# Kernel tuning notes

Hardware: AMD Instinct MI355X
Metric: run time of the kernel (lower is better)

## Reference

```python
import jax, jax.numpy as jnp
import numpy as np

B, C, H, W, WS, SH, NH, P = 64, 512, 28, 28, 7, 3, 16, 10
MLP_H = 2048
EPS = 1e-5
NW = (H // WS) * (W // WS)  # 16 windows per image
N = P + WS * WS             # 59 tokens per window
HEAD_D = C // NH
SCALE = HEAD_D ** -0.5


def _rel_pos_index(ws):
    coords = np.stack(np.meshgrid(np.arange(ws), np.arange(ws), indexing='ij')).reshape(2, -1)
    rel = (coords[:, :, None] - coords[:, None, :]).transpose(1, 2, 0)
    rel[..., 0] += ws - 1
    rel[..., 1] += ws - 1
    rel[..., 0] *= 2 * ws - 1
    return rel.sum(-1)  # (ws*ws, ws*ws)


def _attn_mask(h, w, ws, shift):
    img = np.zeros((h, w), dtype=np.float32)
    slices = (slice(0, -ws), slice(-ws, -shift), slice(-shift, None))
    cnt = 0
    for hs in slices:
        for wsl in slices:
            img[hs, wsl] = cnt
            cnt += 1
    mw = img.reshape(h // ws, ws, w // ws, ws).transpose(0, 2, 1, 3).reshape(-1, ws * ws)
    diff = mw[:, None, :] - mw[:, :, None]
    return np.where(diff != 0, -100.0, 0.0).astype(np.float32)  # (nW, ws*ws, ws*ws)


_RPI = jnp.asarray(_rel_pos_index(WS))
_MASK = jnp.asarray(_attn_mask(H, W, WS, SH))


def _ln(x, g, b):
    mu = jnp.mean(x, -1, keepdims=True)
    var = jnp.mean((x - mu) ** 2, -1, keepdims=True)
    return (x - mu) * jax.lax.rsqrt(var + EPS) * g + b


def _window_partition(x, ws):
    b, h, w, c = x.shape
    x = x.reshape(b, h // ws, ws, w // ws, ws, c).transpose(0, 1, 3, 2, 4, 5)
    return x.reshape(-1, ws, ws, c)


def _window_reverse(win, ws, h, w):
    b = win.shape[0] // ((h // ws) * (w // ws))
    x = win.reshape(b, h // ws, w // ws, ws, ws, -1).transpose(0, 1, 3, 2, 4, 5)
    return x.reshape(b, h, w, -1)


def setup_inputs() -> dict:
    key = jax.random.key(0)
    ks = jax.random.split(key, 8)
    d = {
        'x': jax.random.normal(ks[0], (B, P + H * W, C), jnp.float32),
        'g1': jnp.ones((C,), jnp.float32),
        'b1': jnp.zeros((C,), jnp.float32),
        'qkv_w': jax.random.normal(ks[1], (3 * C, C), jnp.float32) * 0.02,
        'qkv_b': jnp.zeros((3 * C,), jnp.float32),
        'rpb_table': jax.random.normal(ks[2], ((2 * WS - 1) ** 2, NH), jnp.float32) * 0.02,
        'proj_w': jax.random.normal(ks[3], (C, C), jnp.float32) * 0.02,
        'proj_b': jnp.zeros((C,), jnp.float32),
        'g2': jnp.ones((C,), jnp.float32),
        'b2': jnp.zeros((C,), jnp.float32),
        'fc1_w': jax.random.normal(ks[4], (MLP_H, C), jnp.float32) * 0.02,
        'fc1_b': jnp.zeros((MLP_H,), jnp.float32),
        'fc2_w': jax.random.normal(ks[5], (C, MLP_H), jnp.float32) * 0.02,
        'fc2_b': jnp.zeros((C,), jnp.float32),
    }
    return d


def _block(x, g1, b1, qkv_w, qkv_b, rpb_table, proj_w, proj_b, g2, b2, fc1_w, fc1_b, fc2_w, fc2_b):
    prompt = x[:, :P, :]                       # (B, P, C)
    x = x[:, P:, :]                            # (B, H*W, C)
    shortcut = x
    xn = _ln(x, g1, b1).reshape(B, H, W, C)
    # cyclic shift
    xn = jnp.roll(xn, shift=(-SH, -SH), axis=(1, 2))
    xw = _window_partition(xn, WS).reshape(-1, WS * WS, C)  # (B*nW, 49, C)
    # prompt padding (matches torch expand(nW,...).reshape order: index = w*B + b)
    pw = jnp.broadcast_to(prompt[None], (NW, B, P, C)).reshape(-1, P, C)
    xw = jnp.concatenate([pw, xw], axis=1)     # (B*nW, N, C)
    B_ = B * NW
    # attention
    qkv = (xw @ qkv_w.T + qkv_b).reshape(B_, N, 3, NH, HEAD_D).transpose(2, 0, 3, 1, 4)
    q, k, v = qkv[0], qkv[1], qkv[2]
    attn = jnp.einsum('bhnd,bhmd->bhnm', q * SCALE, k)  # (B_, NH, N, N)
    bias = rpb_table[_RPI.reshape(-1)].reshape(WS * WS, WS * WS, NH).transpose(2, 0, 1)
    bias = jnp.pad(bias, ((0, 0), (P, 0), (P, 0)))       # (NH, N, N)
    mask = jnp.pad(_MASK, ((0, 0), (P, 0), (P, 0)))      # (nW, N, N)
    attn = attn + bias[None]
    attn = attn.reshape(B, NW, NH, N, N) + mask[None, :, None]
    attn = jax.nn.softmax(attn.reshape(B_, NH, N, N), axis=-1)
    out = jnp.einsum('bhnm,bhmd->bhnd', attn, v).transpose(0, 2, 1, 3).reshape(B_, N, C)
    out = out @ proj_w.T + proj_b
    # drop prompts, un-window, un-shift
    out = out[:, P:, :].reshape(-1, WS, WS, C)
    xs = _window_reverse(out, WS, H, W)
    xs = jnp.roll(xs, shift=(SH, SH), axis=(1, 2)).reshape(B, H * W, C)
    x = shortcut + xs
    # MLP (exact GELU, as torch nn.GELU)
    h = _ln(x, g2, b2)
    h = jax.nn.gelu(h @ fc1_w.T + fc1_b, approximate=False)
    h = h @ fc2_w.T + fc2_b
    return x + h


def reference(x, g1, b1, qkv_w, qkv_b, rpb_table, proj_w, proj_b, g2, b2, fc1_w, fc1_b, fc2_w, fc2_b):
    return _block(x, g1, b1, qkv_w, qkv_b, rpb_table, proj_w, proj_b, g2, b2, fc1_w, fc1_b, fc2_w, fc2_b)
```

## Files before the change

### kernel.cpp

```cpp
#include <hip/hip_runtime.h>
#include <stdint.h>

typedef unsigned short u16;
typedef unsigned int u32;
typedef __attribute__((ext_vector_type(8))) short short8;
typedef __attribute__((ext_vector_type(4))) float f32x4;

__device__ __forceinline__ u16 f2bf(float f) {
  u32 u = __builtin_bit_cast(u32, f);
  u32 r = u + 0x7FFFu + ((u >> 16) & 1u);
  return (u16)(r >> 16);
}

__device__ __forceinline__ void gl_lds16(const void* g, void* l) {
  __builtin_amdgcn_global_load_lds((__attribute__((address_space(1))) void*)g,
                                   (__attribute__((address_space(3))) void*)l,
                                   16, 0, 0);
}

__device__ __forceinline__ float gelu_fast(float v) {
  float u = 0.7978845608028654f * (v + 0.044715f * v * v * v);
  float a = fabsf(u);
  float e = __expf(-2.0f * a);
  float t = (1.0f - e) / (1.0f + e);
  float th = copysignf(t, u);
  return 0.5f * v * (1.0f + th);
}

__global__ __launch_bounds__(256) void cvt_bf16(const float* __restrict__ in,
                                                u16* __restrict__ out, int n4) {
  int idx = blockIdx.x * 256 + threadIdx.x;
  if (idx < n4) {
    float4 v = ((const float4*)in)[idx];
    u32 lo = (u32)f2bf(v.x) | ((u32)f2bf(v.y) << 16);
    u32 hi = (u32)f2bf(v.z) | ((u32)f2bf(v.w) << 16);
    ((uint2*)out)[idx] = make_uint2(lo, hi);
  }
}

__global__ __launch_bounds__(256) void ln1_kernel(const float* __restrict__ x,
                                                  const float* __restrict__ g,
                                                  const float* __restrict__ bta,
                                                  u16* __restrict__ xcat) {
  int wave = threadIdx.x >> 6, lane = threadIdx.x & 63;
  int row = blockIdx.x * 4 + wave;
  const float* src;
  bool do_ln;
  if (row < 640) {
    int bb = row / 10, p = row - bb * 10;
    src = x + ((size_t)bb * 794 + p) * 512;
    do_ln = false;
  } else {
    int r2 = row - 640;
    int i = r2 / 49, t = r2 - i * 49;
    int bb = i >> 4, nw = i & 15;
    int tr = t / 7, tc = t - tr * 7;
    int hh = (nw >> 2) * 7 + tr + 3; if (hh >= 28) hh -= 28;
    int ww = (nw & 3) * 7 + tc + 3;  if (ww >= 28) ww -= 28;
    src = x + ((size_t)bb * 794 + 10 + hh * 28 + ww) * 512;
    do_ln = true;
  }
  float4 v0 = ((const float4*)src)[lane * 2];
  float4 v1 = ((const float4*)src)[lane * 2 + 1];
  float vals[8] = {v0.x, v0.y, v0.z, v0.w, v1.x, v1.y, v1.z, v1.w};
  u16 ob[8];
  if (do_ln) {
    float s = 0.f, s2 = 0.f;
#pragma unroll
    for (int j = 0; j < 8; ++j) { s += vals[j]; s2 += vals[j] * vals[j]; }
#pragma unroll
    for (int o = 32; o > 0; o >>= 1) { s += __shfl_xor(s, o); s2 += __shfl_xor(s2, o); }
    float mu = s * (1.0f / 512.0f);
    float var = s2 * (1.0f / 512.0f) - mu * mu;
    float inv = rsqrtf(var + 1e-5f);
    float4 ga = ((const float4*)g)[lane * 2], gb = ((const float4*)g)[lane * 2 + 1];
    float4 ba = ((const float4*)bta)[lane * 2], bb2 = ((const float4*)bta)[lane * 2 + 1];
    float gv[8] = {ga.x, ga.y, ga.z, ga.w, gb.x, gb.y, gb.z, gb.w};
    float bv[8] = {ba.x, ba.y, ba.z, ba.w, bb2.x, bb2.y, bb2.z, bb2.w};
#pragma unroll
    for (int j = 0; j < 8; ++j) ob[j] = f2bf((vals[j] - mu) * inv * gv[j] + bv[j]);
  } else {
#pragma unroll
    for (int j = 0; j < 8; ++j) ob[j] = f2bf(vals[j]);
  }
  u32 w0 = (u32)ob[0] | ((u32)ob[1] << 16);
  u32 w1 = (u32)ob[2] | ((u32)ob[3] << 16);
  u32 w2 = (u32)ob[4] | ((u32)ob[5] << 16);
  u32 w3 = (u32)ob[6] | ((u32)ob[7] << 16);
  ((uint4*)(xcat + (size_t)row * 512))[lane] = make_uint4(w0, w1, w2, w3);
}

__global__ __launch_bounds__(256) void ln2_kernel(const float* __restrict__ xn,
                                                  const float* __restrict__ g,
                                                  const float* __restrict__ bta,
                                                  u16* __restrict__ outb) {
  int wave = threadIdx.x >> 6, lane = threadIdx.x & 63;
  size_t row = (size_t)blockIdx.x * 4 + wave;
  const float* src = xn + row * 512;
  float4 v0 = ((const float4*)src)[lane * 2];
  float4 v1 = ((const float4*)src)[lane * 2 + 1];
  float vals[8] = {v0.x, v0.y, v0.z, v0.w, v1.x, v1.y, v1.z, v1.w};
  float s = 0.f, s2 = 0.f;
#pragma unroll
  for (int j = 0; j < 8; ++j) { s += vals[j]; s2 += vals[j] * vals[j]; }
#pragma unroll
  for (int o = 32; o > 0; o >>= 1) { s += __shfl_xor(s, o); s2 += __shfl_xor(s2, o); }
  float mu = s * (1.0f / 512.0f);
  float var = s2 * (1.0f / 512.0f) - mu * mu;
  float inv = rsqrtf(var + 1e-5f);
  float4 ga = ((const float4*)g)[lane * 2], gb = ((const float4*)g)[lane * 2 + 1];
  float4 ba = ((const float4*)bta)[lane * 2], bb2 = ((const float4*)bta)[lane * 2 + 1];
  float gv[8] = {ga.x, ga.y, ga.z, ga.w, gb.x, gb.y, gb.z, gb.w};
  float bv[8] = {ba.x, ba.y, ba.z, ba.w, bb2.x, bb2.y, bb2.z, bb2.w};
  u16 ob[8];
#pragma unroll
  for (int j = 0; j < 8; ++j) ob[j] = f2bf((vals[j] - mu) * inv * gv[j] + bv[j]);
  u32 w0 = (u32)ob[0] | ((u32)ob[1] << 16);
  u32 w1 = (u32)ob[2] | ((u32)ob[3] << 16);
  u32 w2 = (u32)ob[4] | ((u32)ob[5] << 16);
  u32 w3 = (u32)ob[6] | ((u32)ob[7] << 16);
  ((uint4*)(outb + row * 512))[lane] = make_uint4(w0, w1, w2, w3);
}

template <int EPI>
__global__ __launch_bounds__(256) void gemm128d(const u16* __restrict__ A,
                                                const u16* __restrict__ Wt,
                                                const float* __restrict__ bias,
                                                u16* __restrict__ outb,
                                                float* __restrict__ outf,
                                                const float* __restrict__ res,
                                                int M, int N, int K, int Ntiles) {
  __shared__ __align__(16) u16 Asm[2][128 * 32];
  __shared__ __align__(16) u16 Bsm[2][128 * 32];
  const int tid = threadIdx.x;
  const int lane = tid & 63;
  const int wv = tid >> 6;
  const int wm = wv >> 1, wn = wv & 1;
  const int lr = lane & 15;
  const int qh = lane >> 4;
  const int swz8 = (qh ^ ((lr >> 1) & 3)) << 3;

  const int nwg = gridDim.x;
  const int qx = nwg >> 3, rx = nwg & 7;
  const int xcd = blockIdx.x & 7, local = blockIdx.x >> 3;
  const int swz = (xcd < rx ? xcd * (qx + 1) : rx * (qx + 1) + (xcd - rx) * qx) + local;
  const int mt = swz / Ntiles, nt = swz - mt * Ntiles;
  const int tm = mt << 7, tn = nt << 7;

  f32x4 acc[4][4];
#pragma unroll
  for (int m = 0; m < 4; ++m)
#pragma unroll
    for (int n = 0; n < 4; ++n)
#pragma unroll
      for (int e = 0; e < 4; ++e) acc[m][n][e] = 0.f;

  const int sr = tid >> 2;
  const int sl = tid & 3;
  const int scol = (sl ^ ((sr >> 1) & 3)) << 3;
  const u16* Ap0 = A + (size_t)(tm + sr) * K + scol;
  const u16* Ap1 = A + (size_t)(tm + 64 + sr) * K + scol;
  const u16* Bp0 = Wt + (size_t)(tn + sr) * K + scol;
  const u16* Bp1 = Wt + (size_t)(tn + 64 + sr) * K + scol;

#define STAGE(buf, k0)                            \
  do {                                            \
    u16* da = &Asm[buf][tid * 8];                 \
    u16* db = &Bsm[buf][tid * 8];                 \
    gl_lds16(Ap0 + (k0), da);                     \
    gl_lds16(Ap1 + (k0), da + 2048);              \
    gl_lds16(Bp0 + (k0), db);                     \
    gl_lds16(Bp1 + (k0), db + 2048);              \
  } while (0)

  const int NT = K >> 5;
  STAGE(0, 0);

  int cur = 0;
  for (int t = 0; t < NT; ++t) {
    if (t + 1 < NT) {
      STAGE(cur ^ 1, (t + 1) << 5);
      asm volatile("s_waitcnt vmcnt(4)" ::: "memory");
    } else {
      asm volatile("s_waitcnt vmcnt(0)" ::: "memory");
    }
    __builtin_amdgcn_s_barrier();
    asm volatile("" ::: "memory");

    const u16* Ab = &Asm[cur][0];
    const u16* Bb = &Bsm[cur][0];
    short8 av[4], bv[4];
#pragma unroll
    for (int m = 0; m < 4; ++m)
      av[m] = *(const short8*)&Ab[(wm * 64 + m * 16 + lr) * 32 + swz8];
#pragma unroll
    for (int n = 0; n < 4; ++n)
      bv[n] = *(const short8*)&Bb[(wn * 64 + n * 16 + lr) * 32 + swz8];
    __builtin_amdgcn_s_setprio(1);
#pragma unroll
    for (int m = 0; m < 4; ++m)
#pragma unroll
      for (int n = 0; n < 4; ++n)
        acc[m][n] = __builtin_amdgcn_mfma_f32_16x16x32_bf16(av[m], bv[n], acc[m][n], 0, 0, 0);
    __builtin_amdgcn_s_setprio(0);
    asm volatile("" ::: "memory");
    __builtin_amdgcn_s_barrier();
    cur ^= 1;
  }
#undef STAGE

  float bcol[4];
#pragma unroll
  for (int n = 0; n < 4; ++n) bcol[n] = bias[tn + wn * 64 + n * 16 + lr];

#pragma unroll
  for (int m = 0; m < 4; ++m) {
#pragma unroll
    for (int r2 = 0; r2 < 4; ++r2) {
      int grow = tm + wm * 64 + m * 16 + qh * 4 + r2;
      if (EPI == 1) {
        int i = grow / 49, t = grow - i * 49;
        int bb = i >> 4, nw = i & 15;
        int tr = t / 7, tc = t - tr * 7;
        int hh = (nw >> 2) * 7 + tr + 3; if (hh >= 28) hh -= 28;
        int ww = (nw & 3) * 7 + tc + 3;  if (ww >= 28) ww -= 28;
        size_t dstr = ((size_t)bb * 784 + hh * 28 + ww) * 512;
        size_t srcr = ((size_t)bb * 794 + 10 + hh * 28 + ww) * 512;
#pragma unroll
        for (int n = 0; n < 4; ++n) {
          int gcol = tn + wn * 64 + n * 16 + lr;
          float v = acc[m][n][r2] + bcol[n];
          outf[dstr + gcol] = v + res[srcr + gcol];
        }
      } else {
#pragma unroll
        for (int n = 0; n < 4; ++n) {
          int gcol = tn + wn * 64 + n * 16 + lr;
          float v = acc[m][n][r2] + bcol[n];
          if (EPI == 0) {
            outb[(size_t)grow * N + gcol] = f2bf(v);
          } else if (EPI == 2) {
            outb[(size_t)grow * N + gcol] = f2bf(gelu_fast(v));
          } else {
            outf[(size_t)grow * N + gcol] = v + res[(size_t)grow * 512 + gcol];
          }
        }
      }
    }
  }
}

__global__ __launch_bounds__(64) void attn_kernel(const u16* __restrict__ Y,
                                                  const float* __restrict__ rpb,
                                                  u16* __restrict__ outp) {
  __shared__ __align__(16) u16 Plds[64 * 64];
  __shared__ __align__(16) u16 Vt[32 * 64];
  __shared__ float biasl[169];
  const int lane = threadIdx.x;
  const int i = blockIdx.x >> 4;
  const int hd = blockIdx.x & 15;
  const int bp = i & 63;
  const int nw = i & 15;
  const int hi = nw >> 2, wi = nw & 3;
  const int lr = lane & 15;
  const int lk = (lane >> 4) * 8;

  for (int j = lane; j < 169; j += 64) biasl[j] = rpb[j * 16 + hd];

  short8 qf[4], kf[4];
#pragma unroll
  for (int m = 0; m < 4; ++m) {
    int t = m * 16 + lr;
    size_t r = (t < 10) ? (size_t)(bp * 10 + t) : (size_t)(640 + i * 49 + (t - 10));
    const u16* base = Y + r * 1536 + hd * 32 + lk;
    if (t < 59) {
      qf[m] = *(const short8*)(base);
      kf[m] = *(const short8*)(base + 512);
    } else {
#pragma unroll
      for (int e = 0; e < 8; ++e) { qf[m][e] = 0; kf[m][e] = 0; }
    }
  }
  {
    int t = lane;
    if (t < 59) {
      size_t r = (t < 10) ? (size_t)(bp * 10 + t) : (size_t)(640 + i * 49 + (t - 10));
      const u16* vp = Y + r * 1536 + 1024 + hd * 32;
      short8 vv0 = *(const short8*)(vp);
      short8 vv1 = *(const short8*)(vp + 8);
      short8 vv2 = *(const short8*)(vp + 16);
      short8 vv3 = *(const short8*)(vp + 24);
#pragma unroll
      for (int e = 0; e < 8; ++e) {
        Vt[e * 64 + t] = (u16)vv0[e];
        Vt[(8 + e) * 64 + t] = (u16)vv1[e];
        Vt[(16 + e) * 64 + t] = (u16)vv2[e];
        Vt[(24 + e) * 64 + t] = (u16)vv3[e];
      }
    } else {
      for (int d = 0; d < 32; ++d) Vt[d * 64 + t] = 0;
    }
  }

  f32x4 s[4][4];
#pragma unroll
  for (int m = 0; m < 4; ++m)
#pragma unroll
    for (int n = 0; n < 4; ++n)
#pragma unroll
      for (int r2 = 0; r2 < 4; ++r2) s[m][n][r2] = 0.f;
#pragma unroll
  for (int m = 0; m < 4; ++m)
#pragma unroll
    for (int n = 0; n < 4; ++n)
      s[m][n] = __builtin_amdgcn_mfma_f32_16x16x32_bf16(qf[m], kf[n], s[m][n], 0, 0, 0);

  __syncthreads();

  const float SCALE = 0.17677669529663687f;
  const int rgrp = lane >> 4;
#pragma unroll
  for (int m = 0; m < 4; ++m) {
#pragma unroll
    for (int r2 = 0; r2 < 4; ++r2) {
      int rn = m * 16 + rgrp * 4 + r2;
      int qa = rn - 10;
      int qra = qa / 7, qca = qa - qra * 7;
      int regA = 0;
      if (qa >= 0 && qa < 49) {
        int ha = hi * 7 + qra, wa = wi * 7 + qca;
        regA = (ha < 21 ? 0 : (ha < 25 ? 1 : 2)) * 3 + (wa < 21 ? 0 : (wa < 25 ? 1 : 2));
      }
      float vloc[4];
      float mx = -3.0e38f;
#pragma unroll
      for (int n = 0; n < 4; ++n) {
        int cm = n * 16 + lr;
        float v;
        if (cm >= 59) {
          v = -3.0e38f;
        } else {
          v = s[m][n][r2] * SCALE;
          if (rn >= 10 && rn < 59 && cm >= 10) {
            int kb = cm - 10;
            int krb = kb / 7, kcb = kb - krb * 7;
            v += biasl[(qra - krb + 6) * 13 + (qca - kcb + 6)];
            int hb = hi * 7 + krb, wb = wi * 7 + kcb;
            int regB = (hb < 21 ? 0 : (hb < 25 ? 1 : 2)) * 3 + (wb < 21 ? 0 : (wb < 25 ? 1 : 2));
            if (regA != regB) v -= 100.0f;
          }
        }
        vloc[n] = v;
        mx = fmaxf(mx, v);
      }
#pragma unroll
      for (int o = 8; o > 0; o >>= 1) mx = fmaxf(mx, __shfl_xor(mx, o));
      float sum = 0.f;
#pragma unroll
      for (int n = 0; n < 4; ++n) {
        float e = __expf(vloc[n] - mx);
        vloc[n] = e;
        sum += e;
      }
#pragma unroll
      for (int o = 8; o > 0; o >>= 1) sum += __shfl_xor(sum, o);
      float inv = 1.0f / sum;
#pragma unroll
      for (int n = 0; n < 4; ++n)
        Plds[rn * 64 + n * 16 + lr] = f2bf(vloc[n] * inv);
    }
  }

  __syncthreads();

  f32x4 o[4][2];
#pragma unroll
  for (int m = 0; m < 4; ++m)
#pragma unroll
    for (int j = 0; j < 2; ++j)
#pragma unroll
      for (int r2 = 0; r2 < 4; ++r2) o[m][j][r2] = 0.f;
#pragma unroll
  for (int ks = 0; ks < 2; ++ks) {
    short8 pf[4], vf[2];
#pragma unroll
    for (int m = 0; m < 4; ++m)
      pf[m] = *(const short8*)&Plds[(m * 16 + lr) * 64 + ks * 32 + lk];
#pragma unroll
    for (int j = 0; j < 2; ++j)
      vf[j] = *(const short8*)&Vt[(j * 16 + lr) * 64 + ks * 32 + lk];
#pragma unroll
    for (int m = 0; m < 4; ++m)
#pragma unroll
      for (int j = 0; j < 2; ++j)
        o[m][j] = __builtin_amdgcn_mfma_f32_16x16x32_bf16(pf[m], vf[j], o[m][j], 0, 0, 0);
  }

#pragma unroll
  for (int m = 0; m < 4; ++m) {
#pragma unroll
    for (int r2 = 0; r2 < 4; ++r2) {
      int rn = m * 16 + rgrp * 4 + r2;
      if (rn >= 10 && rn < 59) {
        size_t row = (size_t)i * 49 + (rn - 10);
        u16* op = outp + row * 512 + hd * 32;
        op[lr] = f2bf(o[m][0][r2]);
        op[16 + lr] = f2bf(o[m][1][r2]);
      }
    }
  }
}

extern "C" void kernel_launch(void* const* d_in, const int* in_sizes, int n_in,
                              void* d_out, int out_size, void* d_ws, size_t ws_size,
                              hipStream_t stream) {
  const float* x = (const float*)d_in[0];
  const float* g1 = (const float*)d_in[1];
  const float* b1 = (const float*)d_in[2];
  const float* qkv_w = (const float*)d_in[3];
  const float* qkv_b = (const float*)d_in[4];
  const float* rpb = (const float*)d_in[5];
  const float* proj_w = (const float*)d_in[6];
  const float* proj_b = (const float*)d_in[7];
  const float* g2 = (const float*)d_in[8];
  const float* b2 = (const float*)d_in[9];
  const float* fc1_w = (const float*)d_in[10];
  const float* fc1_b = (const float*)d_in[11];
  const float* fc2_w = (const float*)d_in[12];
  const float* fc2_b = (const float*)d_in[13];
  float* out = (float*)d_out;

  char* ws = (char*)d_ws;
  u16* qkv_wb = (u16*)(ws + 0);
  u16* proj_wb = (u16*)(ws + 1572864);
  u16* fc1_wb = (u16*)(ws + 2097152);
  u16* fc2_wb = (u16*)(ws + 4194304);
  u16* xcat = (u16*)(ws + 6291456);
  u16* y = (u16*)(ws + 58327040);
  u16* attnv = (u16*)(ws + 214433792);
  float* xnew = (float*)(ws + 265814016);
  u16* hin = xcat;
  u16* hmid = y;

  cvt_bf16<<<768, 256, 0, stream>>>(qkv_w, qkv_wb, 196608);
  cvt_bf16<<<256, 256, 0, stream>>>(proj_w, proj_wb, 65536);
  cvt_bf16<<<1024, 256, 0, stream>>>(fc1_w, fc1_wb, 262144);
  cvt_bf16<<<1024, 256, 0, stream>>>(fc2_w, fc2_wb, 262144);

  ln1_kernel<<<12704, 256, 0, stream>>>(x, g1, b1, xcat);

  gemm128d<0><<<397 * 12, 256, 0, stream>>>(xcat, qkv_wb, qkv_b, y, nullptr, nullptr,
                                            50816, 1536, 512, 12);

  attn_kernel<<<16384, 64, 0, stream>>>(y, rpb, attnv);

  gemm128d<1><<<392 * 4, 256, 0, stream>>>(attnv, proj_wb, proj_b, nullptr, xnew, x,
                                           50176, 512, 512, 4);

  ln2_kernel<<<12544, 256, 0, stream>>>(xnew, g2, b2, hin);

  gemm128d<2><<<392 * 16, 256, 0, stream>>>(hin, fc1_wb, fc1_b, hmid, nullptr, nullptr,
                                            50176, 2048, 512, 16);

  gemm128d<3><<<392 * 4, 256, 0, stream>>>(hmid, fc2_wb, fc2_b, nullptr, out, xnew,
                                           50176, 512, 2048, 4);
}
```

Baseline: 730.4 us.

## Enlarge GEMM block tile to 256x128 with each wave owning a 64x128 slab

The GEMM kernel's block tile grows from 128x128 to 256x128. Each of the four waves now computes a full 64x128 output slab, so every B fragment read from LDS feeds more MFMAs and the weight tiles are loaded half as often per output. Grid sizes are halved to match. A row guard covers the partial last M tile of the QKV GEMM, whose A loads run past the xcat buffer into other workspace memory. The cost is a doubled accumulator footprint (128 floats per lane) and more LDS per block, which may lower occupancy.

```diff
diff --git a/kernel.cpp b/kernel.cpp
--- a/kernel.cpp
+++ b/kernel.cpp
@@ -123,19 +123,18 @@
 }
 
 template <int EPI>
-__global__ __launch_bounds__(256) void gemm128d(const u16* __restrict__ A,
-                                                const u16* __restrict__ Wt,
-                                                const float* __restrict__ bias,
-                                                u16* __restrict__ outb,
-                                                float* __restrict__ outf,
-                                                const float* __restrict__ res,
-                                                int M, int N, int K, int Ntiles) {
-  __shared__ __align__(16) u16 Asm[2][128 * 32];
+__global__ __launch_bounds__(256) void gemmW(const u16* __restrict__ A,
+                                             const u16* __restrict__ Wt,
+                                             const float* __restrict__ bias,
+                                             u16* __restrict__ outb,
+                                             float* __restrict__ outf,
+                                             const float* __restrict__ res,
+                                             int M, int N, int K, int Ntiles) {
+  __shared__ __align__(16) u16 Asm[2][256 * 32];
   __shared__ __align__(16) u16 Bsm[2][128 * 32];
   const int tid = threadIdx.x;
   const int lane = tid & 63;
   const int wv = tid >> 6;
-  const int wm = wv >> 1, wn = wv & 1;
   const int lr = lane & 15;
   const int qh = lane >> 4;
   const int swz8 = (qh ^ ((lr >> 1) & 3)) << 3;
@@ -145,32 +144,33 @@
   const int xcd = blockIdx.x & 7, local = blockIdx.x >> 3;
   const int swz = (xcd < rx ? xcd * (qx + 1) : rx * (qx + 1) + (xcd - rx) * qx) + local;
   const int mt = swz / Ntiles, nt = swz - mt * Ntiles;
-  const int tm = mt << 7, tn = nt << 7;
-
-  f32x4 acc[4][4];
+  const int tm = mt << 8, tn = nt << 7;
+
+  f32x4 acc[4][8];
 #pragma unroll
   for (int m = 0; m < 4; ++m)
 #pragma unroll
-    for (int n = 0; n < 4; ++n)
+    for (int n = 0; n < 8; ++n)
 #pragma unroll
       for (int e = 0; e < 4; ++e) acc[m][n][e] = 0.f;
 
   const int sr = tid >> 2;
   const int sl = tid & 3;
   const int scol = (sl ^ ((sr >> 1) & 3)) << 3;
-  const u16* Ap0 = A + (size_t)(tm + sr) * K + scol;
-  const u16* Ap1 = A + (size_t)(tm + 64 + sr) * K + scol;
-  const u16* Bp0 = Wt + (size_t)(tn + sr) * K + scol;
-  const u16* Bp1 = Wt + (size_t)(tn + 64 + sr) * K + scol;
+  const u16* Ap = A + (size_t)(tm + sr) * K + scol;
+  const u16* Bp = Wt + (size_t)(tn + sr) * K + scol;
+  const size_t a64 = (size_t)64 * K;
 
 #define STAGE(buf, k0)                            \
   do {                                            \
     u16* da = &Asm[buf][tid * 8];                 \
     u16* db = &Bsm[buf][tid * 8];                 \
-    gl_lds16(Ap0 + (k0), da);                     \
-    gl_lds16(Ap1 + (k0), da + 2048);              \
-    gl_lds16(Bp0 + (k0), db);                     \
-    gl_lds16(Bp1 + (k0), db + 2048);              \
+    gl_lds16(Ap + (k0), da);                      \
+    gl_lds16(Ap + a64 + (k0), da + 2048);         \
+    gl_lds16(Ap + 2 * a64 + (k0), da + 4096);     \
+    gl_lds16(Ap + 3 * a64 + (k0), da + 6144);     \
+    gl_lds16(Bp + (k0), db);                      \
+    gl_lds16(Bp + a64 + (k0), db + 2048);         \
   } while (0)
 
   const int NT = K >> 5;
@@ -180,7 +180,7 @@
   for (int t = 0; t < NT; ++t) {
     if (t + 1 < NT) {
       STAGE(cur ^ 1, (t + 1) << 5);
-      asm volatile("s_waitcnt vmcnt(4)" ::: "memory");
+      asm volatile("s_waitcnt vmcnt(6)" ::: "memory");
     } else {
       asm volatile("s_waitcnt vmcnt(0)" ::: "memory");
     }
@@ -189,18 +189,18 @@
 
     const u16* Ab = &Asm[cur][0];
     const u16* Bb = &Bsm[cur][0];
-    short8 av[4], bv[4];
+    short8 av[4], bv[8];
 #pragma unroll
     for (int m = 0; m < 4; ++m)
-      av[m] = *(const short8*)&Ab[(wm * 64 + m * 16 + lr) * 32 + swz8];
-#pragma unroll
-    for (int n = 0; n < 4; ++n)
-      bv[n] = *(const short8*)&Bb[(wn * 64 + n * 16 + lr) * 32 + swz8];
+      av[m] = *(const short8*)&Ab[(wv * 64 + m * 16 + lr) * 32 + swz8];
+#pragma unroll
+    for (int n = 0; n < 8; ++n)
+      bv[n] = *(const short8*)&Bb[(n * 16 + lr) * 32 + swz8];
     __builtin_amdgcn_s_setprio(1);
 #pragma unroll
     for (int m = 0; m < 4; ++m)
 #pragma unroll
-      for (int n = 0; n < 4; ++n)
+      for (int n = 0; n < 8; ++n)
         acc[m][n] = __builtin_amdgcn_mfma_f32_16x16x32_bf16(av[m], bv[n], acc[m][n], 0, 0, 0);
     __builtin_amdgcn_s_setprio(0);
     asm volatile("" ::: "memory");
@@ -209,15 +209,16 @@
   }
 #undef STAGE
 
-  float bcol[4];
-#pragma unroll
-  for (int n = 0; n < 4; ++n) bcol[n] = bias[tn + wn * 64 + n * 16 + lr];
+  float bcol[8];
+#pragma unroll
+  for (int n = 0; n < 8; ++n) bcol[n] = bias[tn + n * 16 + lr];
 
 #pragma unroll
   for (int m = 0; m < 4; ++m) {
 #pragma unroll
     for (int r2 = 0; r2 < 4; ++r2) {
-      int grow = tm + wm * 64 + m * 16 + qh * 4 + r2;
+      int grow = tm + wv * 64 + m * 16 + qh * 4 + r2;
+      if (grow >= M) continue;
       if (EPI == 1) {
         int i = grow / 49, t = grow - i * 49;
         int bb = i >> 4, nw = i & 15;
@@ -227,15 +228,15 @@
         size_t dstr = ((size_t)bb * 784 + hh * 28 + ww) * 512;
         size_t srcr = ((size_t)bb * 794 + 10 + hh * 28 + ww) * 512;
 #pragma unroll
-        for (int n = 0; n < 4; ++n) {
-          int gcol = tn + wn * 64 + n * 16 + lr;
+        for (int n = 0; n < 8; ++n) {
+          int gcol = tn + n * 16 + lr;
           float v = acc[m][n][r2] + bcol[n];
           outf[dstr + gcol] = v + res[srcr + gcol];
         }
       } else {
 #pragma unroll
-        for (int n = 0; n < 4; ++n) {
-          int gcol = tn + wn * 64 + n * 16 + lr;
+        for (int n = 0; n < 8; ++n) {
+          int gcol = tn + n * 16 + lr;
           float v = acc[m][n][r2] + bcol[n];
           if (EPI == 0) {
             outb[(size_t)grow * N + gcol] = f2bf(v);
@@ -449,19 +450,19 @@
 
   ln1_kernel<<<12704, 256, 0, stream>>>(x, g1, b1, xcat);
 
-  gemm128d<0><<<397 * 12, 256, 0, stream>>>(xcat, qkv_wb, qkv_b, y, nullptr, nullptr,
-                                            50816, 1536, 512, 12);
+  gemmW<0><<<199 * 12, 256, 0, stream>>>(xcat, qkv_wb, qkv_b, y, nullptr, nullptr,
+                                         50816, 1536, 512, 12);
 
   attn_kernel<<<16384, 64, 0, stream>>>(y, rpb, attnv);
 
-  gemm128d<1><<<392 * 4, 256, 0, stream>>>(attnv, proj_wb, proj_b, nullptr, xnew, x,
-                                           50176, 512, 512, 4);
+  gemmW<1><<<196 * 4, 256, 0, stream>>>(attnv, proj_wb, proj_b, nullptr, xnew, x,
+                                        50176, 512, 512, 4);
 
   ln2_kernel<<<12544, 256, 0, stream>>>(xnew, g2, b2, hin);
 
-  gemm128d<2><<<392 * 16, 256, 0, stream>>>(hin, fc1_wb, fc1_b, hmid, nullptr, nullptr,
-                                            50176, 2048, 512, 16);
-
-  gemm128d<3><<<392 * 4, 256, 0, stream>>>(hmid, fc2_wb, fc2_b, nullptr, out, xnew,
-                                           50176, 512, 2048, 4);
-}
+  gemmW<2><<<196 * 16, 256, 0, stream>>>(hin, fc1_wb, fc1_b, hmid, nullptr, nullptr,
+                                         50176, 2048, 512, 16);
+
+  gemmW<3><<<196 * 4, 256, 0, stream>>>(hmid, fc2_wb, fc2_b, nullptr, out, xnew,
+                                        50176, 512, 2048, 4);
+}
```

Result: slower. 1.138 ms (+55.8%).

## Load GEMM weight fragments directly from global memory, dropping B LDS staging

Applied to the files above, without the earlier changes.

The GEMM kernel no longer stages the weight (B) tile through shared memory. Each wave now loads its four 16x32 B fragments directly from global memory into registers every K-step, which halves LDS usage and enables a launch-bounds occupancy hint of 3 blocks. The wait counts are adjusted to cover the extra outstanding vector loads. In exchange, B data is no longer shared between the two wm waves through LDS, so each is re-fetched from global memory or L2. The per-lane global reads are 16-byte strided rows, and the B loads have no prefetch ahead of use.

```diff
diff --git a/kernel.cpp b/kernel.cpp
--- a/kernel.cpp
+++ b/kernel.cpp
@@ -123,15 +123,14 @@
 }
 
 template <int EPI>
-__global__ __launch_bounds__(256) void gemm128d(const u16* __restrict__ A,
-                                                const u16* __restrict__ Wt,
-                                                const float* __restrict__ bias,
-                                                u16* __restrict__ outb,
-                                                float* __restrict__ outf,
-                                                const float* __restrict__ res,
-                                                int M, int N, int K, int Ntiles) {
+__global__ __launch_bounds__(256, 3) void gemm128b(const u16* __restrict__ A,
+                                                   const u16* __restrict__ Wt,
+                                                   const float* __restrict__ bias,
+                                                   u16* __restrict__ outb,
+                                                   float* __restrict__ outf,
+                                                   const float* __restrict__ res,
+                                                   int M, int N, int K, int Ntiles) {
   __shared__ __align__(16) u16 Asm[2][128 * 32];
-  __shared__ __align__(16) u16 Bsm[2][128 * 32];
   const int tid = threadIdx.x;
   const int lane = tid & 63;
   const int wv = tid >> 6;
@@ -160,54 +159,60 @@
   const int scol = (sl ^ ((sr >> 1) & 3)) << 3;
   const u16* Ap0 = A + (size_t)(tm + sr) * K + scol;
   const u16* Ap1 = A + (size_t)(tm + 64 + sr) * K + scol;
-  const u16* Bp0 = Wt + (size_t)(tn + sr) * K + scol;
-  const u16* Bp1 = Wt + (size_t)(tn + 64 + sr) * K + scol;
-
-#define STAGE(buf, k0)                            \
+
+  const u16* Bq = Wt + (size_t)(tn + wn * 64 + lr) * K + qh * 8;
+  const size_t bstep = (size_t)16 * K;
+  const u16* Bq0 = Bq;
+  const u16* Bq1 = Bq + bstep;
+  const u16* Bq2 = Bq + 2 * bstep;
+  const u16* Bq3 = Bq + 3 * bstep;
+
+#define STAGE_A(buf, k0)                          \
   do {                                            \
     u16* da = &Asm[buf][tid * 8];                 \
-    u16* db = &Bsm[buf][tid * 8];                 \
     gl_lds16(Ap0 + (k0), da);                     \
     gl_lds16(Ap1 + (k0), da + 2048);              \
-    gl_lds16(Bp0 + (k0), db);                     \
-    gl_lds16(Bp1 + (k0), db + 2048);              \
   } while (0)
 
   const int NT = K >> 5;
-  STAGE(0, 0);
+  STAGE_A(0, 0);
 
   int cur = 0;
   for (int t = 0; t < NT; ++t) {
+    const int k0e = t << 5;
+    short8 bv0 = *(const short8*)(Bq0 + k0e);
+    short8 bv1 = *(const short8*)(Bq1 + k0e);
+    short8 bv2 = *(const short8*)(Bq2 + k0e);
+    short8 bv3 = *(const short8*)(Bq3 + k0e);
+    asm volatile("" ::: "memory");
     if (t + 1 < NT) {
-      STAGE(cur ^ 1, (t + 1) << 5);
+      STAGE_A(cur ^ 1, (t + 1) << 5);
+      asm volatile("s_waitcnt vmcnt(6)" ::: "memory");
+    } else {
       asm volatile("s_waitcnt vmcnt(4)" ::: "memory");
-    } else {
-      asm volatile("s_waitcnt vmcnt(0)" ::: "memory");
     }
     __builtin_amdgcn_s_barrier();
     asm volatile("" ::: "memory");
 
     const u16* Ab = &Asm[cur][0];
-    const u16* Bb = &Bsm[cur][0];
-    short8 av[4], bv[4];
+    short8 av[4];
 #pragma unroll
     for (int m = 0; m < 4; ++m)
       av[m] = *(const short8*)&Ab[(wm * 64 + m * 16 + lr) * 32 + swz8];
-#pragma unroll
-    for (int n = 0; n < 4; ++n)
-      bv[n] = *(const short8*)&Bb[(wn * 64 + n * 16 + lr) * 32 + swz8];
     __builtin_amdgcn_s_setprio(1);
 #pragma unroll
-    for (int m = 0; m < 4; ++m)
-#pragma unroll
-      for (int n = 0; n < 4; ++n)
-        acc[m][n] = __builtin_amdgcn_mfma_f32_16x16x32_bf16(av[m], bv[n], acc[m][n], 0, 0, 0);
+    for (int m = 0; m < 4; ++m) {
+      acc[m][0] = __builtin_amdgcn_mfma_f32_16x16x32_bf16(av[m], bv0, acc[m][0], 0, 0, 0);
+      acc[m][1] = __builtin_amdgcn_mfma_f32_16x16x32_bf16(av[m], bv1, acc[m][1], 0, 0, 0);
+      acc[m][2] = __builtin_amdgcn_mfma_f32_16x16x32_bf16(av[m], bv2, acc[m][2], 0, 0, 0);
+      acc[m][3] = __builtin_amdgcn_mfma_f32_16x16x32_bf16(av[m], bv3, acc[m][3], 0, 0, 0);
+    }
     __builtin_amdgcn_s_setprio(0);
     asm volatile("" ::: "memory");
     __builtin_amdgcn_s_barrier();
     cur ^= 1;
   }
-#undef STAGE
+#undef STAGE_A
 
   float bcol[4];
 #pragma unroll
@@ -449,19 +454,19 @@
 
   ln1_kernel<<<12704, 256, 0, stream>>>(x, g1, b1, xcat);
 
-  gemm128d<0><<<397 * 12, 256, 0, stream>>>(xcat, qkv_wb, qkv_b, y, nullptr, nullptr,
+  gemm128b<0><<<397 * 12, 256, 0, stream>>>(xcat, qkv_wb, qkv_b, y, nullptr, nullptr,
                                             50816, 1536, 512, 12);
 
   attn_kernel<<<16384, 64, 0, stream>>>(y, rpb, attnv);
 
-  gemm128d<1><<<392 * 4, 256, 0, stream>>>(attnv, proj_wb, proj_b, nullptr, xnew, x,
+  gemm128b<1><<<392 * 4, 256, 0, stream>>>(attnv, proj_wb, proj_b, nullptr, xnew, x,
                                            50176, 512, 512, 4);
 
   ln2_kernel<<<12544, 256, 0, stream>>>(xnew, g2, b2, hin);
 
-  gemm128d<2><<<392 * 16, 256, 0, stream>>>(hin, fc1_wb, fc1_b, hmid, nullptr, nullptr,
+  gemm128b<2><<<392 * 16, 256, 0, stream>>>(hin, fc1_wb, fc1_b, hmid, nullptr, nullptr,
                                             50176, 2048, 512, 16);
 
-  gemm128d<3><<<392 * 4, 256, 0, stream>>>(hmid, fc2_wb, fc2_b, nullptr, out, xnew,
+  gemm128b<3><<<392 * 4, 256, 0, stream>>>(hmid, fc2_wb, fc2_b, nullptr, out, xnew,
                                            50176, 512, 2048, 4);
 }
```

Result: slower. 953.1 us (+30.5%).
